# Kernel tuning notes

Hardware: AMD Instinct MI355X
Metric: run time of the kernel (lower is better)

## Reference

```python
import jax, jax.numpy as jnp
import numpy as np

EPS = 1e-6
SLOPE = 0.01  # torch LeakyReLU / VNLeakyReLU default negative_slope
B = 1024      # number of graphs (segments)
N, S, V, H = 120000, 256, 64, 64


def _vn(W, x):
    # VNLinear: channel-mixing linear on (N, C, 3) vector features, W: (O, C)
    return jnp.einsum('oc,ncd->nod', W, x)


def _gv_linear(Wv1, Wv2, Ws, Wg, bg, sca, vec):
    # GVLinear: vec -> hidden vec, concat |vec| with sca, gate out_vec by sigmoid(out_sca)
    vi = _vn(Wv1, vec)                                   # (N, Hid, 3)
    vnorm = jnp.linalg.norm(vi, axis=-1)                 # (N, Hid)
    out_sca = jnp.concatenate([vnorm, sca], axis=-1) @ Ws.T   # (N, out_sca)
    out_vec = _vn(Wv2, vi)                               # (N, out_vec, 3)
    gate = jax.nn.sigmoid(out_sca @ Wg.T + bg)[..., None]
    return out_sca, gate * out_vec


def _vn_lrelu(Wd, x):
    # VNLeakyReLU: direction-gated leaky relu on vector channels
    d = _vn(Wd, x)
    dot = jnp.sum(x * d, axis=-1, keepdims=True)
    dsq = jnp.sum(d * d, axis=-1, keepdims=True)
    mask = (dot >= 0).astype(x.dtype)
    proj = x - (dot / (dsq + EPS)) * d
    return SLOPE * x + (1.0 - SLOPE) * (mask * x + (1.0 - mask) * proj)


def _lrelu(x):
    return jnp.where(x >= 0, x, SLOPE * x)


def setup_inputs() -> dict:
    key = jax.random.key(0)
    ks = jax.random.split(key, 40)
    g = lambda i, shape, s=1.0: jax.random.normal(ks[i], shape, dtype=jnp.float32) * s
    w = 0.06  # ~1/sqrt(fan_in) for fan_in 256-320
    inp = {
        'h_sca': g(0, (N, S)),
        'h_vec': g(1, (N, V, 3)),
        'pos_context': g(2, (N, 3), 3.0),
        'time_embed': g(3, (100, S), 0.05),
        # att_net: GVPerceptronVN(256,64 -> 256,64)
        'att1_Wv1': g(4, (H, V), 0.12), 'att1_Wv2': g(5, (H, H), 0.12),
        'att1_Ws': g(6, (S, S + H), w), 'att1_Wg': g(7, (H, S), w), 'att1_bg': g(8, (H,), 0.01),
        'att1_Wd': g(9, (H, H), 0.12),
        # att_net: GVLinear(256,64 -> 1,1), dim_hid = max(64,1) = 64
        'att2_Wv1': g(10, (H, H), 0.12), 'att2_Wv2': g(11, (1, H), 0.12),
        'att2_Ws': g(12, (1, S + H), w), 'att2_Wg': g(13, (1, 1), 0.5), 'att2_bg': g(14, (1,), 0.01),
        # net: GVPerceptronVN(256,64 -> 256,64)
        'net1_Wv1': g(15, (H, V), 0.12), 'net1_Wv2': g(16, (H, H), 0.12),
        'net1_Ws': g(17, (S, S + H), w), 'net1_Wg': g(18, (H, S), w), 'net1_bg': g(19, (H,), 0.01),
        'net1_Wd': g(20, (H, H), 0.12),
        # net: GVLinear(256,64 -> 256,64)
        'net2_Wv1': g(21, (H, H), 0.12), 'net2_Wv2': g(22, (S - (S - V), H), 0.12).reshape(V, H),
        'net2_Ws': g(23, (S, S + H), w), 'net2_Wg': g(24, (V, S), w), 'net2_bg': g(25, (V,), 0.01),
        't': 17,
        'batch_id': jnp.sort(jax.random.randint(ks[30], (N,), 0, B)),
    }
    return inp


def reference(h_sca, h_vec, pos_context, time_embed,
              att1_Wv1, att1_Wv2, att1_Ws, att1_Wg, att1_bg, att1_Wd,
              att2_Wv1, att2_Wv2, att2_Ws, att2_Wg, att2_bg,
              net1_Wv1, net1_Wv2, net1_Ws, net1_Wg, net1_bg, net1_Wd,
              net2_Wv1, net2_Wv2, net2_Ws, net2_Wg, net2_bg,
              t, batch_id):
    sca = h_sca + time_embed[t]          # same timestep embedding broadcast to all N nodes
    vec = h_vec

    # attention branch: GVPerceptronVN -> GVLinear(...,1,1), keep scalar output
    s, v = _gv_linear(att1_Wv1, att1_Wv2, att1_Ws, att1_Wg, att1_bg, sca, vec)
    s, v = _lrelu(s), _vn_lrelu(att1_Wd, v)
    att, _ = _gv_linear(att2_Wv1, att2_Wv2, att2_Ws, att2_Wg, att2_bg, s, v)  # (N,1)

    # feature branch: GVPerceptronVN -> GVLinear(...,in_sca,in_vec)
    s2, v2 = _gv_linear(net1_Wv1, net1_Wv2, net1_Ws, net1_Wg, net1_bg, sca, vec)
    s2, v2 = _lrelu(s2), _vn_lrelu(net1_Wd, v2)
    fs, fv = _gv_linear(net2_Wv1, net2_Wv2, net2_Ws, net2_Wg, net2_bg, s2, v2)

    # scatter_softmax over batch_id segments
    m = jax.ops.segment_max(att, batch_id, num_segments=B)
    e = jnp.exp(att - m[batch_id])
    z = jax.ops.segment_sum(e, batch_id, num_segments=B)
    w = e / z[batch_id]                  # (N,1)

    pos_focal = jax.ops.segment_sum(w * pos_context, batch_id, num_segments=B)   # (B,3)
    feat_focal = jax.ops.segment_sum(w * fs, batch_id, num_segments=B)           # (B,256)
    vec_focal = jax.ops.segment_sum(w[:, :, None] * fv, batch_id, num_segments=B)  # (B,64,3)
    return feat_focal, vec_focal, pos_focal
```

## Files before the change

### kernel.cpp

```cpp
#include <hip/hip_runtime.h>
#include <math.h>

#define NN 120000
#define NT 32
#define TPB 512
#define NBLK (NN / NT)
#define BSEG 1024

typedef __attribute__((ext_vector_type(8))) short short8;
typedef __attribute__((ext_vector_type(16))) float floatx16;

#define OFF_A1_WV1 0
#define OFF_A1_WV2 4096
#define OFF_A1_WS  8192
#define OFF_A1_WG  90112
#define OFF_A1_WD  106496
#define OFF_A2_WV1 110592
#define OFF_N1_WV1 114688
#define OFF_N1_WV2 118784
#define OFF_N1_WS  122880
#define OFF_N1_WG  204800
#define OFF_N1_WD  221184
#define OFF_N2_WV1 225280
#define OFF_N2_WV2 229376
#define OFF_N2_WS  233472
#define OFF_N2_WG  315392
#define W_TOTAL    331776

__device__ __forceinline__ unsigned short f2bf(float x) {
  unsigned int u = __float_as_uint(x);
  u += 0x7FFFu + ((u >> 16) & 1u);
  return (unsigned short)(u >> 16);
}
__device__ __forceinline__ float bf2f(unsigned short h) {
  return __uint_as_float(((unsigned int)h) << 16);
}

struct P {
  const float *h_sca, *h_vec, *pos, *te;
  const float *a1_bg, *n1_bg, *n2_bg, *a2_Ws;
  const int *t, *bid;
  const unsigned short* wb;
  float *att, *w, *out;
};


struct CvtP { const float* src[15]; unsigned short* dst; };

__global__ __launch_bounds__(256) void cvt_kernel(CvtP c) {
  const int sizes[15] = {4096, 4096, 81920, 16384, 4096, 4096,
                         4096, 4096, 81920, 16384, 4096,
                         4096, 4096, 81920, 16384};
  int idx = blockIdx.x * 256 + threadIdx.x;
  if (idx >= W_TOTAL) return;
  int seg = 0, off = 0;
  while (idx - off >= sizes[seg]) { off += sizes[seg]; ++seg; }
  c.dst[idx] = f2bf(c.src[seg][idx - off]);
}


__device__ __forceinline__ void stage(const P& p, unsigned short* sS, unsigned short* sV,
                                      const float* te_row, int node0, int tid) {
  {
    int i = tid >> 4, c0 = (tid & 15) * 16;
    const float4* src = (const float4*)&p.h_sca[(node0 + i) * 256 + c0];
    const float4* te4 = (const float4*)&te_row[c0];
    unsigned int* dst = (unsigned int*)&sS[i * 264 + c0];
#pragma unroll
    for (int v = 0; v < 4; ++v) {
      float4 a = src[v], b = te4[v];
      dst[v * 2 + 0] = (unsigned int)f2bf(a.x + b.x) | ((unsigned int)f2bf(a.y + b.y) << 16);
      dst[v * 2 + 1] = (unsigned int)f2bf(a.z + b.z) | ((unsigned int)f2bf(a.w + b.w) << 16);
    }
  }
  for (int q4 = tid; q4 < NT * 48; q4 += TPB) {
    float4 v = *(const float4*)&p.h_vec[node0 * 192 + q4 * 4];
    const float* vv = (const float*)&v;
#pragma unroll
    for (int e = 0; e < 4; ++e) {
      int qq = q4 * 4 + e;
      int i = qq / 192, r = qq - i * 192, c = r / 3, d = r - c * 3;
      sV[(i * 3 + d) * 72 + c] = f2bf(vv[e]);
    }
  }
}

__device__ __forceinline__ void big_gemm(const unsigned short* __restrict__ Wb,
                                         const unsigned short* sVN,
                                         const unsigned short* sX,
                                         unsigned short* sDst,
                                         int wid, int lane) {
  const int m = lane & 31, h = lane >> 5;
  const int n0 = wid * 32;
  const unsigned short* wrow = Wb + (n0 + m) * 320 + h * 8;
  floatx16 acc0 = {}, acc1 = {};
#pragma unroll
  for (int k = 0; k < 20; k += 2) {
    short8 a0, a1;
    if (k < 4)     a0 = *(const short8*)&sVN[m * 72 + k * 16 + h * 8];
    else           a0 = *(const short8*)&sX[m * 264 + (k - 4) * 16 + h * 8];
    if (k + 1 < 4) a1 = *(const short8*)&sVN[m * 72 + (k + 1) * 16 + h * 8];
    else           a1 = *(const short8*)&sX[m * 264 + (k - 3) * 16 + h * 8];
    short8 b0 = *(const short8*)&wrow[k * 16];
    short8 b1 = *(const short8*)&wrow[k * 16 + 16];
    acc0 = __builtin_amdgcn_mfma_f32_32x32x16_bf16(a0, b0, acc0, 0, 0, 0);
    acc1 = __builtin_amdgcn_mfma_f32_32x32x16_bf16(a1, b1, acc1, 0, 0, 0);
  }
  __syncthreads();
#pragma unroll
  for (int r = 0; r < 16; ++r) {
    int row = (r & 3) + 8 * (r >> 2) + 4 * h;
    sDst[row * 264 + n0 + m] = f2bf(acc0[r] + acc1[r]);
  }
}

__device__ __forceinline__ void gate_gemm(const unsigned short* __restrict__ Wg,
                                          const float* __restrict__ bg,
                                          const unsigned short* sX,
                                          unsigned short* sG, int wid, int lane) {
  const int m = lane & 31, h = lane >> 5;
  const int n0 = wid * 32;
  const unsigned short* wrow = Wg + (n0 + m) * 256 + h * 8;
  floatx16 acc0 = {}, acc1 = {};
#pragma unroll
  for (int k = 0; k < 16; k += 2) {
    short8 a0 = *(const short8*)&sX[m * 264 + k * 16 + h * 8];
    short8 a1 = *(const short8*)&sX[m * 264 + k * 16 + 16 + h * 8];
    short8 b0 = *(const short8*)&wrow[k * 16];
    short8 b1 = *(const short8*)&wrow[k * 16 + 16];
    acc0 = __builtin_amdgcn_mfma_f32_32x32x16_bf16(a0, b0, acc0, 0, 0, 0);
    acc1 = __builtin_amdgcn_mfma_f32_32x32x16_bf16(a1, b1, acc1, 0, 0, 0);
  }
  float bb = bg[n0 + m];
#pragma unroll
  for (int r = 0; r < 16; ++r) {
    int i = (r & 3) + 8 * (r >> 2) + 4 * h;
    float v = acc0[r] + acc1[r] + bb;
    sG[i * 64 + n0 + m] = f2bf(1.f / (1.f + __expf(-v)));
  }
}

__device__ __forceinline__ void vecmm(const unsigned short* __restrict__ Wb,
                                      const unsigned short* sSrc,
                                      unsigned short* sDst,
                                      const unsigned short* sGA,
                                      const unsigned short* sGD,
                                      int wid, int lane) {
  if (wid >= 6) return;
  const int m = lane & 31, h = lane >> 5;
  const int nd0 = (wid >> 1) * 32, o0 = (wid & 1) * 32;
  const unsigned short* wrow = Wb + (o0 + m) * 64 + h * 8;
  short8 b0 = *(const short8*)&wrow[0];
  short8 b1 = *(const short8*)&wrow[16];
  short8 b2 = *(const short8*)&wrow[32];
  short8 b3 = *(const short8*)&wrow[48];
  const int gi = (nd0 + m) / 3;
  floatx16 acc = {};
#pragma unroll
  for (int k0 = 0; k0 < 64; k0 += 16) {
    short8 a = *(const short8*)&sSrc[(nd0 + m) * 72 + k0 + h * 8];
    if (sGA) {
#pragma unroll
      for (int j = 0; j < 8; ++j)
        a[j] = (short)f2bf(bf2f((unsigned short)a[j]) * bf2f(sGA[gi * 64 + k0 + h * 8 + j]));
    }
    short8 b = (k0 == 0) ? b0 : (k0 == 16) ? b1 : (k0 == 32) ? b2 : b3;
    acc = __builtin_amdgcn_mfma_f32_32x32x16_bf16(a, b, acc, 0, 0, 0);
  }
#pragma unroll
  for (int r = 0; r < 16; ++r) {
    int nd = nd0 + (r & 3) + 8 * (r >> 2) + 4 * h;
    float v = acc[r];
    if (sGD) v *= bf2f(sGD[(nd / 3) * 64 + o0 + m]);
    sDst[nd * 72 + o0 + m] = f2bf(v);
  }
}

__device__ __forceinline__ void vnorm(const unsigned short* sV, unsigned short* sVN, int tid) {
  for (int qq = tid; qq < NT * 64; qq += TPB) {
    int i = qq >> 6, c = qq & 63;
    float x = bf2f(sV[(i * 3 + 0) * 72 + c]);
    float y = bf2f(sV[(i * 3 + 1) * 72 + c]);
    float z = bf2f(sV[(i * 3 + 2) * 72 + c]);
    sVN[i * 72 + c] = f2bf(sqrtf(x * x + y * y + z * z));
  }
}

__device__ __forceinline__ void vn_lrelu(unsigned short* sVx, const unsigned short* sVd,
                                         const unsigned short* sG, int tid) {
  for (int qq = tid; qq < NT * 64; qq += TPB) {
    int i = qq >> 6, c = qq & 63;
    float g = bf2f(sG[i * 64 + c]);
    int bx = (i * 3) * 72 + c;
    float x0 = bf2f(sVx[bx]) * g, x1 = bf2f(sVx[bx + 72]) * g, x2 = bf2f(sVx[bx + 144]) * g;
    float d0 = bf2f(sVd[bx]), d1 = bf2f(sVd[bx + 72]), d2 = bf2f(sVd[bx + 144]);
    float dot = x0 * d0 + x1 * d1 + x2 * d2;
    float dsq = d0 * d0 + d1 * d1 + d2 * d2;
    float f = dot >= 0.f ? 0.f : 0.99f * dot / (dsq + 1e-6f);
    sVx[bx]       = f2bf(x0 - f * d0);
    sVx[bx + 72]  = f2bf(x1 - f * d1);
    sVx[bx + 144] = f2bf(x2 - f * d2);
  }
}

__device__ __forceinline__ void lrelu_vec(unsigned short* sS, int u, int nthr) {
  for (int cc = u; cc < NT * 32; cc += nthr) {
    int i = cc >> 5, off = (cc & 31) * 8;
    short8 v = *(short8*)&sS[i * 264 + off];
#pragma unroll
    for (int j = 0; j < 8; ++j) {
      float x = bf2f((unsigned short)v[j]);
      v[j] = (short)f2bf(x >= 0.f ? x : 0.01f * x);
    }
    *(short8*)&sS[i * 264 + off] = v;
  }
}

__device__ __forceinline__ float* out_addr(float* out, int b, int f) {
  if (f < 256) return out + b * 256 + f;
  if (f < 448) return out + 1024 * 256 + b * 192 + (f - 256);
  return out + 1024 * 256 + 1024 * 192 + b * 3 + (f - 448);
}


__global__ __launch_bounds__(TPB, 6) void att_kernel(P p) {
  __shared__ unsigned short sS[NT * 264];
  __shared__ unsigned short sVA[96 * 72], sVB[96 * 72];
  __shared__ unsigned short sGN[2304];
  unsigned short* sVN = sGN;
  unsigned short* sG = sGN;
  int tid = threadIdx.x, wid = tid >> 6, lane = tid & 63;
  int node0 = blockIdx.x * NT;
  const unsigned short* wb = p.wb;

  stage(p, sS, sVA, p.te + p.t[0] * 256, node0, tid); __syncthreads();
  vecmm(wb + OFF_A1_WV1, sVA, sVB, nullptr, nullptr, wid, lane); __syncthreads();
  vnorm(sVB, sVN, tid); __syncthreads();
  big_gemm(wb + OFF_A1_WS, sVN, sS, sS, wid, lane); __syncthreads();
  if (wid < 2) gate_gemm(wb + OFF_A1_WG, p.a1_bg, sS, sG, wid, lane);
  else vecmm(wb + OFF_A1_WV2, sVB, sVA, nullptr, nullptr, wid - 2, lane);
  __syncthreads();
  vecmm(wb + OFF_A1_WD, sVA, sVB, sG, nullptr, wid, lane); __syncthreads();
  vn_lrelu(sVA, sVB, sG, tid); __syncthreads();
  vecmm(wb + OFF_A2_WV1, sVA, sVB, nullptr, nullptr, wid, lane); __syncthreads();

  int i = tid >> 4, j = tid & 15;
  float part = 0.f;
#pragma unroll
  for (int cc = 0; cc < 4; ++cc) {
    int c = j + cc * 16;
    float x = bf2f(sVB[(i * 3 + 0) * 72 + c]);
    float y = bf2f(sVB[(i * 3 + 1) * 72 + c]);
    float z = bf2f(sVB[(i * 3 + 2) * 72 + c]);
    part = fmaf(p.a2_Ws[c], sqrtf(x * x + y * y + z * z), part);
  }
  for (int k = j; k < 256; k += 16) {
    float x = bf2f(sS[i * 264 + k]);
    x = x >= 0.f ? x : 0.01f * x;
    part = fmaf(p.a2_Ws[64 + k], x, part);
  }
  part += __shfl_down(part, 8, 16);
  part += __shfl_down(part, 4, 16);
  part += __shfl_down(part, 2, 16);
  part += __shfl_down(part, 1, 16);
  if (j == 0) p.att[node0 + i] = part;
}


__global__ __launch_bounds__(256) void softmax_kernel(const float* __restrict__ att,
                                                      const int* __restrict__ bid,
                                                      float* __restrict__ w) {
  __shared__ float red[256];
  __shared__ float s_m, s_z;
  int b = blockIdx.x, tid = threadIdx.x;
  int lo = 0, hi = NN;
  while (lo < hi) { int mid = (lo + hi) >> 1; if (bid[mid] < b) lo = mid + 1; else hi = mid; }
  int start = lo;
  hi = NN;
  while (lo < hi) { int mid = (lo + hi) >> 1; if (bid[mid] < b + 1) lo = mid + 1; else hi = mid; }
  int end = lo;

  float m = -1e30f;
  for (int i = start + tid; i < end; i += 256) m = fmaxf(m, att[i]);
  red[tid] = m; __syncthreads();
  for (int s = 128; s > 0; s >>= 1) { if (tid < s) red[tid] = fmaxf(red[tid], red[tid + s]); __syncthreads(); }
  if (tid == 0) s_m = red[0];
  __syncthreads();
  m = s_m;
  float z = 0.f;
  for (int i = start + tid; i < end; i += 256) z += __expf(att[i] - m);
  red[tid] = z; __syncthreads();
  for (int s = 128; s > 0; s >>= 1) { if (tid < s) red[tid] += red[tid + s]; __syncthreads(); }
  if (tid == 0) s_z = red[0];
  __syncthreads();
  float inv = 1.f / s_z;
  for (int i = start + tid; i < end; i += 256) w[i] = __expf(att[i] - m) * inv;
}


__global__ __launch_bounds__(TPB, 6) void net_kernel(P p) {
  __shared__ unsigned short sS[NT * 264];
  __shared__ unsigned short sVA[96 * 72], sVB[96 * 72];
  __shared__ unsigned short sGN[2304];
  __shared__ float s_w[NT];
  __shared__ float s_pos[NT * 3];
  __shared__ int s_bid[NT];
  unsigned short* sVN = sGN;
  unsigned short* sG = sGN;
  int tid = threadIdx.x, wid = tid >> 6, lane = tid & 63;
  int node0 = blockIdx.x * NT;
  const unsigned short* wb = p.wb;

  stage(p, sS, sVA, p.te + p.t[0] * 256, node0, tid); __syncthreads();
  vecmm(wb + OFF_N1_WV1, sVA, sVB, nullptr, nullptr, wid, lane); __syncthreads();
  vnorm(sVB, sVN, tid); __syncthreads();
  big_gemm(wb + OFF_N1_WS, sVN, sS, sS, wid, lane); __syncthreads();
  if (wid < 2) gate_gemm(wb + OFF_N1_WG, p.n1_bg, sS, sG, wid, lane);
  else vecmm(wb + OFF_N1_WV2, sVB, sVA, nullptr, nullptr, wid - 2, lane);
  __syncthreads();
  if (wid < 6) vecmm(wb + OFF_N1_WD, sVA, sVB, sG, nullptr, wid, lane);
  else lrelu_vec(sS, tid - 384, 128);
  __syncthreads();
  vn_lrelu(sVA, sVB, sG, tid); __syncthreads();
  vecmm(wb + OFF_N2_WV1, sVA, sVB, nullptr, nullptr, wid, lane); __syncthreads();
  vnorm(sVB, sVN, tid); __syncthreads();
  big_gemm(wb + OFF_N2_WS, sVN, sS, sS, wid, lane); __syncthreads();
  if (wid < 2) gate_gemm(wb + OFF_N2_WG, p.n2_bg, sS, sG, wid, lane);
  else if (wid < 8 && wid >= 2) {
    vecmm(wb + OFF_N2_WV2, sVB, sVA, nullptr, nullptr, wid - 2, lane);
    if (wid >= 7) {
      int u = tid - 448;
      if (u < NT) { s_w[u] = p.w[node0 + u]; s_bid[u] = p.bid[node0 + u]; }
      for (int v = u; v < NT * 3; v += 64) s_pos[v] = p.pos[node0 * 3 + v];
    }
  }
  __syncthreads();

  if (tid < 451) {
    int f = tid;
    float acc = 0.f;
    int cur = s_bid[0];
    int c = 0, d = 0;
    if (f >= 256 && f < 448) { int r = f - 256; c = r / 3; d = r - c * 3; }
    for (int i2 = 0; i2 < NT; ++i2) {
      int sg = s_bid[i2];
      if (sg != cur) { atomicAdd(out_addr(p.out, cur, f), acc); acc = 0.f; cur = sg; }
      float val;
      if (f < 256) val = bf2f(sS[i2 * 264 + f]);
      else if (f < 448)
        val = bf2f(sVA[(i2 * 3 + d) * 72 + c]) * bf2f(sG[i2 * 64 + c]);
      else val = s_pos[i2 * 3 + (f - 448)];
      acc = fmaf(s_w[i2], val, acc);
    }
    atomicAdd(out_addr(p.out, cur, f), acc);
  }
}


extern "C" void kernel_launch(void* const* d_in, const int* in_sizes, int n_in,
                              void* d_out, int out_size, void* d_ws, size_t ws_size,
                              hipStream_t stream) {
  float* ws = (float*)d_ws;
  unsigned short* wb = (unsigned short*)(ws + 2 * NN);

  CvtP c;
  c.src[0]  = (const float*)d_in[4];
  c.src[1]  = (const float*)d_in[5];
  c.src[2]  = (const float*)d_in[6];
  c.src[3]  = (const float*)d_in[7];
  c.src[4]  = (const float*)d_in[9];
  c.src[5]  = (const float*)d_in[10];
  c.src[6]  = (const float*)d_in[15];
  c.src[7]  = (const float*)d_in[16];
  c.src[8]  = (const float*)d_in[17];
  c.src[9]  = (const float*)d_in[18];
  c.src[10] = (const float*)d_in[20];
  c.src[11] = (const float*)d_in[21];
  c.src[12] = (const float*)d_in[22];
  c.src[13] = (const float*)d_in[23];
  c.src[14] = (const float*)d_in[24];
  c.dst = wb;

  P p;
  p.h_sca = (const float*)d_in[0];
  p.h_vec = (const float*)d_in[1];
  p.pos   = (const float*)d_in[2];
  p.te    = (const float*)d_in[3];
  p.a1_bg = (const float*)d_in[8];
  p.a2_Ws = (const float*)d_in[12];
  p.n1_bg = (const float*)d_in[19];
  p.n2_bg = (const float*)d_in[25];
  p.t   = (const int*)d_in[26];
  p.bid = (const int*)d_in[27];
  p.wb  = wb;
  p.att = ws;
  p.w   = ws + NN;
  p.out = (float*)d_out;

  hipMemsetAsync(d_out, 0, (size_t)out_size * sizeof(float), stream);
  cvt_kernel<<<(W_TOTAL + 255) / 256, 256, 0, stream>>>(c);
  att_kernel<<<NBLK, TPB, 0, stream>>>(p);
  softmax_kernel<<<BSEG, 256, 0, stream>>>(p.att, p.bid, p.w);
  net_kernel<<<NBLK, TPB, 0, stream>>>(p);
}
```

Measured before the change: 685.3 us.

## Vectorize elementwise stages, split gate multiply from vecmm, use native bf16 conversion

```diff
diff --git a/kernel.cpp b/kernel.cpp
--- a/kernel.cpp
+++ b/kernel.cpp
@@ -1,4 +1,5 @@
 #include <hip/hip_runtime.h>
+#include <hip/hip_bf16.h>
 #include <math.h>
 
 #define NN 120000
@@ -28,13 +29,17 @@
 #define W_TOTAL    331776
 
 __device__ __forceinline__ unsigned short f2bf(float x) {
-  unsigned int u = __float_as_uint(x);
-  u += 0x7FFFu + ((u >> 16) & 1u);
-  return (unsigned short)(u >> 16);
+  __hip_bfloat16 b = __float2bfloat16(x);
+  return __builtin_bit_cast(unsigned short, b);
+}
+__device__ __forceinline__ unsigned int f2bf2(float lo, float hi) {
+  return (unsigned int)f2bf(lo) | ((unsigned int)f2bf(hi) << 16);
 }
 __device__ __forceinline__ float bf2f(unsigned short h) {
   return __uint_as_float(((unsigned int)h) << 16);
 }
+__device__ __forceinline__ float bflo(unsigned int u) { return __uint_as_float(u << 16); }
+__device__ __forceinline__ float bfhi(unsigned int u) { return __uint_as_float(u & 0xffff0000u); }
 
 struct P {
   const float *h_sca, *h_vec, *pos, *te;
@@ -61,27 +66,30 @@
 
 __device__ __forceinline__ void stage(const P& p, unsigned short* sS, unsigned short* sV,
                                       const float* te_row, int node0, int tid) {
+  int i = tid >> 4, j = tid & 15;
   {
-    int i = tid >> 4, c0 = (tid & 15) * 16;
+    int c0 = j * 16;
     const float4* src = (const float4*)&p.h_sca[(node0 + i) * 256 + c0];
     const float4* te4 = (const float4*)&te_row[c0];
-    unsigned int* dst = (unsigned int*)&sS[i * 264 + c0];
-#pragma unroll
-    for (int v = 0; v < 4; ++v) {
-      float4 a = src[v], b = te4[v];
-      dst[v * 2 + 0] = (unsigned int)f2bf(a.x + b.x) | ((unsigned int)f2bf(a.y + b.y) << 16);
-      dst[v * 2 + 1] = (unsigned int)f2bf(a.z + b.z) | ((unsigned int)f2bf(a.w + b.w) << 16);
-    }
-  }
-  for (int q4 = tid; q4 < NT * 48; q4 += TPB) {
-    float4 v = *(const float4*)&p.h_vec[node0 * 192 + q4 * 4];
-    const float* vv = (const float*)&v;
-#pragma unroll
-    for (int e = 0; e < 4; ++e) {
-      int qq = q4 * 4 + e;
-      int i = qq / 192, r = qq - i * 192, c = r / 3, d = r - c * 3;
-      sV[(i * 3 + d) * 72 + c] = f2bf(vv[e]);
-    }
+    float4 a0 = src[0], b0 = te4[0];
+    float4 a1 = src[1], b1 = te4[1];
+    float4 a2 = src[2], b2 = te4[2];
+    float4 a3 = src[3], b3 = te4[3];
+    uint4 o0 = make_uint4(f2bf2(a0.x + b0.x, a0.y + b0.y), f2bf2(a0.z + b0.z, a0.w + b0.w),
+                          f2bf2(a1.x + b1.x, a1.y + b1.y), f2bf2(a1.z + b1.z, a1.w + b1.w));
+    uint4 o1 = make_uint4(f2bf2(a2.x + b2.x, a2.y + b2.y), f2bf2(a2.z + b2.z, a2.w + b2.w),
+                          f2bf2(a3.x + b3.x, a3.y + b3.y), f2bf2(a3.z + b3.z, a3.w + b3.w));
+    *(uint4*)&sS[i * 264 + c0] = o0;
+    *(uint4*)&sS[i * 264 + c0 + 8] = o1;
+  }
+  {
+    int c0 = j * 4;
+    const float4* src = (const float4*)&p.h_vec[(node0 + i) * 192 + c0 * 3];
+    float4 v0 = src[0], v1 = src[1], v2 = src[2];
+    int b = (i * 3) * 72 + c0;
+    *(uint2*)&sV[b]       = make_uint2(f2bf2(v0.x, v0.w), f2bf2(v1.z, v2.y));
+    *(uint2*)&sV[b + 72]  = make_uint2(f2bf2(v0.y, v1.x), f2bf2(v1.w, v2.z));
+    *(uint2*)&sV[b + 144] = make_uint2(f2bf2(v0.z, v1.y), f2bf2(v2.x, v2.w));
   }
 }
 
@@ -136,15 +144,13 @@
   for (int r = 0; r < 16; ++r) {
     int i = (r & 3) + 8 * (r >> 2) + 4 * h;
     float v = acc0[r] + acc1[r] + bb;
-    sG[i * 64 + n0 + m] = f2bf(1.f / (1.f + __expf(-v)));
+    sG[i * 64 + n0 + m] = f2bf(__builtin_amdgcn_rcpf(1.f + __expf(-v)));
   }
 }
 
 __device__ __forceinline__ void vecmm(const unsigned short* __restrict__ Wb,
                                       const unsigned short* sSrc,
                                       unsigned short* sDst,
-                                      const unsigned short* sGA,
-                                      const unsigned short* sGD,
                                       int wid, int lane) {
   if (wid >= 6) return;
   const int m = lane & 31, h = lane >> 5;
@@ -154,65 +160,103 @@
   short8 b1 = *(const short8*)&wrow[16];
   short8 b2 = *(const short8*)&wrow[32];
   short8 b3 = *(const short8*)&wrow[48];
-  const int gi = (nd0 + m) / 3;
   floatx16 acc = {};
 #pragma unroll
   for (int k0 = 0; k0 < 64; k0 += 16) {
     short8 a = *(const short8*)&sSrc[(nd0 + m) * 72 + k0 + h * 8];
-    if (sGA) {
-#pragma unroll
-      for (int j = 0; j < 8; ++j)
-        a[j] = (short)f2bf(bf2f((unsigned short)a[j]) * bf2f(sGA[gi * 64 + k0 + h * 8 + j]));
-    }
     short8 b = (k0 == 0) ? b0 : (k0 == 16) ? b1 : (k0 == 32) ? b2 : b3;
     acc = __builtin_amdgcn_mfma_f32_32x32x16_bf16(a, b, acc, 0, 0, 0);
   }
 #pragma unroll
   for (int r = 0; r < 16; ++r) {
     int nd = nd0 + (r & 3) + 8 * (r >> 2) + 4 * h;
-    float v = acc[r];
-    if (sGD) v *= bf2f(sGD[(nd / 3) * 64 + o0 + m]);
-    sDst[nd * 72 + o0 + m] = f2bf(v);
+    sDst[nd * 72 + o0 + m] = f2bf(acc[r]);
   }
 }
 
 __device__ __forceinline__ void vnorm(const unsigned short* sV, unsigned short* sVN, int tid) {
-  for (int qq = tid; qq < NT * 64; qq += TPB) {
-    int i = qq >> 6, c = qq & 63;
-    float x = bf2f(sV[(i * 3 + 0) * 72 + c]);
-    float y = bf2f(sV[(i * 3 + 1) * 72 + c]);
-    float z = bf2f(sV[(i * 3 + 2) * 72 + c]);
-    sVN[i * 72 + c] = f2bf(sqrtf(x * x + y * y + z * z));
-  }
-}
-
-__device__ __forceinline__ void vn_lrelu(unsigned short* sVx, const unsigned short* sVd,
-                                         const unsigned short* sG, int tid) {
-  for (int qq = tid; qq < NT * 64; qq += TPB) {
-    int i = qq >> 6, c = qq & 63;
-    float g = bf2f(sG[i * 64 + c]);
-    int bx = (i * 3) * 72 + c;
-    float x0 = bf2f(sVx[bx]) * g, x1 = bf2f(sVx[bx + 72]) * g, x2 = bf2f(sVx[bx + 144]) * g;
-    float d0 = bf2f(sVd[bx]), d1 = bf2f(sVd[bx + 72]), d2 = bf2f(sVd[bx + 144]);
-    float dot = x0 * d0 + x1 * d1 + x2 * d2;
-    float dsq = d0 * d0 + d1 * d1 + d2 * d2;
-    float f = dot >= 0.f ? 0.f : 0.99f * dot / (dsq + 1e-6f);
-    sVx[bx]       = f2bf(x0 - f * d0);
-    sVx[bx + 72]  = f2bf(x1 - f * d1);
-    sVx[bx + 144] = f2bf(x2 - f * d2);
-  }
+  if (tid >= 256) return;
+  int i = tid >> 3, c0 = (tid & 7) * 8;
+  int b = (i * 3) * 72 + c0;
+  short8 vx = *(const short8*)&sV[b];
+  short8 vy = *(const short8*)&sV[b + 72];
+  short8 vz = *(const short8*)&sV[b + 144];
+  unsigned int o[4];
+#pragma unroll
+  for (int q = 0; q < 4; ++q) {
+    float x0 = bf2f((unsigned short)vx[2 * q]),     y0 = bf2f((unsigned short)vy[2 * q]),     z0 = bf2f((unsigned short)vz[2 * q]);
+    float x1 = bf2f((unsigned short)vx[2 * q + 1]), y1 = bf2f((unsigned short)vy[2 * q + 1]), z1 = bf2f((unsigned short)vz[2 * q + 1]);
+    o[q] = f2bf2(sqrtf(x0 * x0 + y0 * y0 + z0 * z0), sqrtf(x1 * x1 + y1 * y1 + z1 * z1));
+  }
+  *(uint4*)&sVN[i * 72 + c0] = make_uint4(o[0], o[1], o[2], o[3]);
+}
+
+__device__ __forceinline__ void gatemul(unsigned short* sVx, const unsigned short* sG, int tid) {
+  if (tid >= 256) return;
+  int i = tid >> 3, c0 = (tid & 7) * 8;
+  short8 g = *(const short8*)&sG[i * 64 + c0];
+  float gf[8];
+#pragma unroll
+  for (int j = 0; j < 8; ++j) gf[j] = bf2f((unsigned short)g[j]);
+  int b = (i * 3) * 72 + c0;
+#pragma unroll
+  for (int d = 0; d < 3; ++d) {
+    short8 v = *(const short8*)&sVx[b + d * 72];
+    unsigned int o[4];
+#pragma unroll
+    for (int q = 0; q < 4; ++q)
+      o[q] = f2bf2(bf2f((unsigned short)v[2 * q]) * gf[2 * q],
+                   bf2f((unsigned short)v[2 * q + 1]) * gf[2 * q + 1]);
+    *(uint4*)&sVx[b + d * 72] = make_uint4(o[0], o[1], o[2], o[3]);
+  }
+}
+
+__device__ __forceinline__ void vn_lrelu(unsigned short* sVx, const unsigned short* sVd, int tid) {
+  if (tid >= 256) return;
+  int i = tid >> 3, c0 = (tid & 7) * 8;
+  int b = (i * 3) * 72 + c0;
+  short8 x0 = *(const short8*)&sVx[b];
+  short8 x1 = *(const short8*)&sVx[b + 72];
+  short8 x2 = *(const short8*)&sVx[b + 144];
+  short8 d0 = *(const short8*)&sVd[b];
+  short8 d1 = *(const short8*)&sVd[b + 72];
+  short8 d2 = *(const short8*)&sVd[b + 144];
+  float rx[8], ry[8], rz[8];
+#pragma unroll
+  for (int j = 0; j < 8; ++j) {
+    float a0 = bf2f((unsigned short)x0[j]), a1 = bf2f((unsigned short)x1[j]), a2 = bf2f((unsigned short)x2[j]);
+    float e0 = bf2f((unsigned short)d0[j]), e1 = bf2f((unsigned short)d1[j]), e2 = bf2f((unsigned short)d2[j]);
+    float dot = a0 * e0 + a1 * e1 + a2 * e2;
+    float dsq = e0 * e0 + e1 * e1 + e2 * e2;
+    float f = dot >= 0.f ? 0.f : 0.99f * dot * __builtin_amdgcn_rcpf(dsq + 1e-6f);
+    rx[j] = a0 - f * e0; ry[j] = a1 - f * e1; rz[j] = a2 - f * e2;
+  }
+  unsigned int ox[4], oy[4], oz[4];
+#pragma unroll
+  for (int q = 0; q < 4; ++q) {
+    ox[q] = f2bf2(rx[2 * q], rx[2 * q + 1]);
+    oy[q] = f2bf2(ry[2 * q], ry[2 * q + 1]);
+    oz[q] = f2bf2(rz[2 * q], rz[2 * q + 1]);
+  }
+  *(uint4*)&sVx[b]       = make_uint4(ox[0], ox[1], ox[2], ox[3]);
+  *(uint4*)&sVx[b + 72]  = make_uint4(oy[0], oy[1], oy[2], oy[3]);
+  *(uint4*)&sVx[b + 144] = make_uint4(oz[0], oz[1], oz[2], oz[3]);
 }
 
 __device__ __forceinline__ void lrelu_vec(unsigned short* sS, int u, int nthr) {
   for (int cc = u; cc < NT * 32; cc += nthr) {
     int i = cc >> 5, off = (cc & 31) * 8;
     short8 v = *(short8*)&sS[i * 264 + off];
-#pragma unroll
-    for (int j = 0; j < 8; ++j) {
-      float x = bf2f((unsigned short)v[j]);
-      v[j] = (short)f2bf(x >= 0.f ? x : 0.01f * x);
+    unsigned int o[4];
+#pragma unroll
+    for (int q = 0; q < 4; ++q) {
+      float a = bf2f((unsigned short)v[2 * q]);
+      float b = bf2f((unsigned short)v[2 * q + 1]);
+      a = a >= 0.f ? a : 0.01f * a;
+      b = b >= 0.f ? b : 0.01f * b;
+      o[q] = f2bf2(a, b);
     }
-    *(short8*)&sS[i * 264 + off] = v;
+    *(uint4*)&sS[i * 264 + off] = make_uint4(o[0], o[1], o[2], o[3]);
   }
 }
 
@@ -234,30 +278,54 @@
   const unsigned short* wb = p.wb;
 
   stage(p, sS, sVA, p.te + p.t[0] * 256, node0, tid); __syncthreads();
-  vecmm(wb + OFF_A1_WV1, sVA, sVB, nullptr, nullptr, wid, lane); __syncthreads();
+  vecmm(wb + OFF_A1_WV1, sVA, sVB, wid, lane); __syncthreads();
   vnorm(sVB, sVN, tid); __syncthreads();
   big_gemm(wb + OFF_A1_WS, sVN, sS, sS, wid, lane); __syncthreads();
   if (wid < 2) gate_gemm(wb + OFF_A1_WG, p.a1_bg, sS, sG, wid, lane);
-  else vecmm(wb + OFF_A1_WV2, sVB, sVA, nullptr, nullptr, wid - 2, lane);
-  __syncthreads();
-  vecmm(wb + OFF_A1_WD, sVA, sVB, sG, nullptr, wid, lane); __syncthreads();
-  vn_lrelu(sVA, sVB, sG, tid); __syncthreads();
-  vecmm(wb + OFF_A2_WV1, sVA, sVB, nullptr, nullptr, wid, lane); __syncthreads();
+  else vecmm(wb + OFF_A1_WV2, sVB, sVA, wid - 2, lane);
+  __syncthreads();
+  gatemul(sVA, sG, tid); __syncthreads();
+  vecmm(wb + OFF_A1_WD, sVA, sVB, wid, lane); __syncthreads();
+  vn_lrelu(sVA, sVB, tid); __syncthreads();
+  vecmm(wb + OFF_A2_WV1, sVA, sVB, wid, lane); __syncthreads();
 
   int i = tid >> 4, j = tid & 15;
   float part = 0.f;
-#pragma unroll
-  for (int cc = 0; cc < 4; ++cc) {
-    int c = j + cc * 16;
-    float x = bf2f(sVB[(i * 3 + 0) * 72 + c]);
-    float y = bf2f(sVB[(i * 3 + 1) * 72 + c]);
-    float z = bf2f(sVB[(i * 3 + 2) * 72 + c]);
-    part = fmaf(p.a2_Ws[c], sqrtf(x * x + y * y + z * z), part);
-  }
-  for (int k = j; k < 256; k += 16) {
-    float x = bf2f(sS[i * 264 + k]);
-    x = x >= 0.f ? x : 0.01f * x;
-    part = fmaf(p.a2_Ws[64 + k], x, part);
+  {
+    int c0 = j * 4;
+    uint2 wx = *(const uint2*)&sVB[(i * 3 + 0) * 72 + c0];
+    uint2 wy = *(const uint2*)&sVB[(i * 3 + 1) * 72 + c0];
+    uint2 wz = *(const uint2*)&sVB[(i * 3 + 2) * 72 + c0];
+    float4 ws = *(const float4*)&p.a2_Ws[c0];
+    float n0 = sqrtf(bflo(wx.x) * bflo(wx.x) + bflo(wy.x) * bflo(wy.x) + bflo(wz.x) * bflo(wz.x));
+    float n1 = sqrtf(bfhi(wx.x) * bfhi(wx.x) + bfhi(wy.x) * bfhi(wy.x) + bfhi(wz.x) * bfhi(wz.x));
+    float n2 = sqrtf(bflo(wx.y) * bflo(wx.y) + bflo(wy.y) * bflo(wy.y) + bflo(wz.y) * bflo(wz.y));
+    float n3 = sqrtf(bfhi(wx.y) * bfhi(wx.y) + bfhi(wy.y) * bfhi(wy.y) + bfhi(wz.y) * bfhi(wz.y));
+    part = fmaf(ws.x, n0, part);
+    part = fmaf(ws.y, n1, part);
+    part = fmaf(ws.z, n2, part);
+    part = fmaf(ws.w, n3, part);
+  }
+  {
+    int k0 = j * 16;
+    short8 s0 = *(const short8*)&sS[i * 264 + k0];
+    short8 s1 = *(const short8*)&sS[i * 264 + k0 + 8];
+    const float4* wp = (const float4*)&p.a2_Ws[64 + k0];
+#pragma unroll
+    for (int q = 0; q < 4; ++q) {
+      float4 w4 = wp[q];
+      float vv[4];
+#pragma unroll
+      for (int e = 0; e < 4; ++e) {
+        short raw = (q < 2) ? ((q == 0) ? s0[e] : s0[4 + e]) : ((q == 2) ? s1[e] : s1[4 + e]);
+        float x = bf2f((unsigned short)raw);
+        vv[e] = x >= 0.f ? x : 0.01f * x;
+      }
+      part = fmaf(w4.x, vv[0], part);
+      part = fmaf(w4.y, vv[1], part);
+      part = fmaf(w4.z, vv[2], part);
+      part = fmaf(w4.w, vv[3], part);
+    }
   }
   part += __shfl_down(part, 8, 16);
   part += __shfl_down(part, 4, 16);
@@ -312,28 +380,28 @@
   const unsigned short* wb = p.wb;
 
   stage(p, sS, sVA, p.te + p.t[0] * 256, node0, tid); __syncthreads();
-  vecmm(wb + OFF_N1_WV1, sVA, sVB, nullptr, nullptr, wid, lane); __syncthreads();
+  vecmm(wb + OFF_N1_WV1, sVA, sVB, wid, lane);
+  if (wid >= 6) {
+    int u = tid - 384;
+    if (u < NT) { s_w[u] = p.w[node0 + u]; s_bid[u] = p.bid[node0 + u]; }
+    for (int v = u; v < NT * 3; v += 128) s_pos[v] = p.pos[node0 * 3 + v];
+  }
+  __syncthreads();
   vnorm(sVB, sVN, tid); __syncthreads();
   big_gemm(wb + OFF_N1_WS, sVN, sS, sS, wid, lane); __syncthreads();
   if (wid < 2) gate_gemm(wb + OFF_N1_WG, p.n1_bg, sS, sG, wid, lane);
-  else vecmm(wb + OFF_N1_WV2, sVB, sVA, nullptr, nullptr, wid - 2, lane);
-  __syncthreads();
-  if (wid < 6) vecmm(wb + OFF_N1_WD, sVA, sVB, sG, nullptr, wid, lane);
-  else lrelu_vec(sS, tid - 384, 128);
-  __syncthreads();
-  vn_lrelu(sVA, sVB, sG, tid); __syncthreads();
-  vecmm(wb + OFF_N2_WV1, sVA, sVB, nullptr, nullptr, wid, lane); __syncthreads();
+  else vecmm(wb + OFF_N1_WV2, sVB, sVA, wid - 2, lane);
+  __syncthreads();
+  if (tid < 256) gatemul(sVA, sG, tid);
+  else lrelu_vec(sS, tid - 256, 256);
+  __syncthreads();
+  vecmm(wb + OFF_N1_WD, sVA, sVB, wid, lane); __syncthreads();
+  vn_lrelu(sVA, sVB, tid); __syncthreads();
+  vecmm(wb + OFF_N2_WV1, sVA, sVB, wid, lane); __syncthreads();
   vnorm(sVB, sVN, tid); __syncthreads();
   big_gemm(wb + OFF_N2_WS, sVN, sS, sS, wid, lane); __syncthreads();
   if (wid < 2) gate_gemm(wb + OFF_N2_WG, p.n2_bg, sS, sG, wid, lane);
-  else if (wid < 8 && wid >= 2) {
-    vecmm(wb + OFF_N2_WV2, sVB, sVA, nullptr, nullptr, wid - 2, lane);
-    if (wid >= 7) {
-      int u = tid - 448;
-      if (u < NT) { s_w[u] = p.w[node0 + u]; s_bid[u] = p.bid[node0 + u]; }
-      for (int v = u; v < NT * 3; v += 64) s_pos[v] = p.pos[node0 * 3 + v];
-    }
-  }
+  else vecmm(wb + OFF_N2_WV2, sVB, sVA, wid - 2, lane);
   __syncthreads();
 
   if (tid < 451) {
```

Measured after the change: 658.8 us. 1.04x faster.
